# Kernel optimization log

Measured on AMD Instinct MI355X. Metric: run time of the kernel, lower is better.

The kernel has to match this reference:

```python
import jax, jax.numpy as jnp
import numpy as np

# Config mirrors Voxelization(__init__) with training=True -> max_voxels[0]
VOXEL_SIZE = (0.05, 0.05, 0.1)
PC_LO = (0.0, -40.0, -3.0)
PC_HI = (70.4, 40.0, 1.0)
MAX_POINTS = 64
MAX_VOXELS = 60000
GX = int(round((PC_HI[0] - PC_LO[0]) / VOXEL_SIZE[0]))  # 1408
GY = int(round((PC_HI[1] - PC_LO[1]) / VOXEL_SIZE[1]))  # 1600
GZ = int(round((PC_HI[2] - PC_LO[2]) / VOXEL_SIZE[2]))  # 40
SENT = GX * GY * GZ  # sentinel linear id for out-of-range points


def setup_inputs() -> dict:
    key = jax.random.key(0)
    u = jax.random.uniform(key, (2_000_000, 4), dtype=jnp.float32)
    lo = jnp.array([PC_LO[0], PC_LO[1], PC_LO[2], 0.0], jnp.float32)
    span = jnp.array([PC_HI[0] - PC_LO[0], PC_HI[1] - PC_LO[1], PC_HI[2] - PC_LO[2], 1.0], jnp.float32)
    points = lo + u * span  # xyz inside range, intensity in [0,1)
    return {"points": points}


def _voxelize(points):
    N, C = points.shape
    vs = jnp.array(VOXEL_SIZE, jnp.float32)
    lo = jnp.array(PC_LO, jnp.float32)
    grid = jnp.array([GX, GY, GZ], jnp.int32)

    g = jnp.floor((points[:, :3] - lo) / vs).astype(jnp.int32)  # [N,3] grid coords (x,y,z)
    valid = jnp.all((g >= 0) & (g < grid), axis=1)
    lin = (g[:, 0] * GY + g[:, 1]) * GZ + g[:, 2]
    lin = jnp.where(valid, lin, SENT).astype(jnp.int32)

    # Stable sort by voxel id; ties keep original point order (deterministic mode)
    order = jnp.argsort(lin)  # jnp.argsort is stable
    sl = lin[order]
    idx = jnp.arange(N, dtype=jnp.int32)
    is_start = jnp.concatenate([jnp.ones((1,), bool), sl[1:] != sl[:-1]])
    gid_sorted = (jnp.cumsum(is_start) - 1).astype(jnp.int32)  # sorted-group id per sorted point

    # First original point index per group -> first-occurrence voxel ordering
    group_first = jnp.full((N,), N, jnp.int32).at[gid_sorted].min(
        jnp.where(is_start, order.astype(jnp.int32), N))
    group_lin = jnp.full((N,), SENT, jnp.int32).at[gid_sorted].min(sl)
    group_first = jnp.where(group_lin == SENT, N, group_first)  # sentinel group ranks last
    perm = jnp.argsort(group_first)  # rank -> group
    inv_rank = jnp.zeros((N,), jnp.int32).at[perm].set(idx)  # group -> rank

    num_valid = jnp.sum(is_start & (sl != SENT)).astype(jnp.int32)
    voxel_num = jnp.minimum(num_valid, MAX_VOXELS)

    # Position within voxel (point order within group)
    start_idx = jax.lax.cummax(jnp.where(is_start, idx, -1))
    pos_sorted = idx - start_idx

    gid = jnp.zeros((N,), jnp.int32).at[order].set(gid_sorted)
    pos = jnp.zeros((N,), jnp.int32).at[order].set(pos_sorted)
    rank = inv_rank[gid]
    keep = valid & (rank < MAX_VOXELS) & (pos < MAX_POINTS)
    rk = jnp.where(keep, rank, MAX_VOXELS)  # OOB -> dropped
    pk = jnp.where(keep, pos, MAX_POINTS)

    voxels = jnp.zeros((MAX_VOXELS, MAX_POINTS, C), points.dtype).at[rk, pk].set(points, mode='drop')
    coors = jnp.zeros((MAX_VOXELS, 3), jnp.int32).at[rk].set(g[:, ::-1], mode='drop')  # flip -> (z,y,x)
    group_count = jnp.zeros((N,), jnp.int32).at[gid_sorted].add((sl != SENT).astype(jnp.int32))
    npv = jnp.minimum(group_count[perm], MAX_POINTS)[:MAX_VOXELS].astype(jnp.int32)
    return voxels, coors, npv, voxel_num


def reference(points):
    # Padded equivalent of torch output (voxels[:n], coors[:n].flip(-1), npv[:n]):
    # rows >= voxel_num are zero; voxel_num gives the true count.
    return _voxelize(points)
```

## Files before the change

### kernel.cpp

```cpp
#include <hip/hip_runtime.h>


#define MAXV 60000
#define MAXP 64
#define FCUT 131072
#define NBUCK 512
#define BSHIFT 13
#define BSLOTS 8192
#define TMASK (NBUCK * BSLOTS - 1)
#define BCAP 5120
#define ECAP 512
#define BIN_CHUNK 4096
#define BIN_T 512
#define NZ 512
#define CHUNK 2048
#define NCHUNK (FCUT / CHUNK)

typedef unsigned long long u64;

__device__ __forceinline__ int compute_lin(float x, float y, float z) {
  float fx = floorf((x - 0.0f) / 0.05f);
  float fy = floorf((y - (-40.0f)) / 0.05f);
  float fz = floorf((z - (-3.0f)) / 0.1f);
  if (!(fx >= 0.0f && fx < 1408.0f &&
        fy >= 0.0f && fy < 1600.0f &&
        fz >= 0.0f && fz < 40.0f))
    return -1;
  return (((int)fx) * 1600 + (int)fy) * 40 + (int)fz;
}

__device__ __forceinline__ unsigned hash_s(int lin) {
  unsigned h = (unsigned)lin * 2654435761u;
  return (h ^ (h >> 15)) & TMASK;
}

__global__ __launch_bounds__(BIN_T) void k_binA(
    const float4* __restrict__ pts, int N, u64* __restrict__ binned,
    int* __restrict__ bucketCnt, int nBin,
    float4* __restrict__ zOut, int nf4, float* __restrict__ zTail, int ntail,
    ulonglong2* __restrict__ zFs, int nfs2) {
  int tid = threadIdx.x;

  if (blockIdx.x >= nBin) {
    int gid = (blockIdx.x - nBin) * BIN_T + tid;
    int stride = NZ * BIN_T;
    float4 z = make_float4(0.f, 0.f, 0.f, 0.f);
    for (int i = gid; i < nf4; i += stride) zOut[i] = z;
    for (int i = gid; i < nfs2; i += stride) zFs[i] = make_ulonglong2(0, 0);
    if (gid < ntail) zTail[gid] = 0.f;
    return;
  }

  __shared__ int hist[NBUCK];
  __shared__ int lbase[NBUCK];
  __shared__ int cursor[NBUCK];
  __shared__ int gbase[NBUCK];
  __shared__ int totSh;
  __shared__ u64 stage[BIN_CHUNK];

  int blockStart = blockIdx.x * BIN_CHUNK;
  hist[tid] = 0;
  __syncthreads();

  unsigned sArr[8];
  int linArr[8];
#pragma unroll
  for (int j = 0; j < 8; j++) {
    int i = blockStart + j * BIN_T + tid;
    unsigned sv = 0xFFFFFFFFu; int lv = 0;
    if (i < N) {
      float4 p = pts[i];
      int lin = compute_lin(p.x, p.y, p.z);
      if (lin >= 0) {
        sv = hash_s(lin);
        lv = lin;
        atomicAdd(&hist[sv >> BSHIFT], 1);
      }
    }
    sArr[j] = sv; linArr[j] = lv;
  }
  __syncthreads();

  int v = hist[tid];
  lbase[tid] = v;
  __syncthreads();
  for (int off = 1; off < NBUCK; off <<= 1) {
    int t = (tid >= off) ? lbase[tid - off] : 0;
    __syncthreads();
    lbase[tid] += t;
    __syncthreads();
  }
  int excl = lbase[tid] - v;
  __syncthreads();
  lbase[tid] = excl;
  cursor[tid] = excl;
  __syncthreads();

#pragma unroll
  for (int j = 0; j < 8; j++) {
    if (sArr[j] != 0xFFFFFFFFu) {
      int b = (int)(sArr[j] >> BSHIFT);
      int k = atomicAdd(&cursor[b], 1);
      int i = blockStart + j * BIN_T + tid;
      stage[k] = ((u64)(unsigned)linArr[j] << 32) | (unsigned)i;
    }
  }
  __syncthreads();

  int cntB = cursor[tid] - lbase[tid];
  if (cntB > 0) gbase[tid] = atomicAdd(&bucketCnt[tid], cntB);
  if (tid == BIN_T - 1) totSh = cursor[NBUCK - 1];
  __syncthreads();

  int tot = totSh;
  for (int k = tid; k < tot; k += BIN_T) {
    u64 e = stage[k];
    int b = (int)(hash_s((int)(e >> 32)) >> BSHIFT);
    int off = gbase[b] + (k - lbase[b]);
    if (off < BCAP) binned[(size_t)b * BCAP + off] = e;
  }
}

__global__ __launch_bounds__(1024) void k_binB(
    const u64* __restrict__ binned, const int* __restrict__ bucketCnt,
    u64* __restrict__ fs, u64* __restrict__ gEbuf, int* __restrict__ bcnt,
    int* __restrict__ occPartials) {
  __shared__ u64 tab[BSLOTS];
  __shared__ u64 ev[ECAP];
  __shared__ int evCnt;
  __shared__ int occTot;

  int tid = threadIdx.x;
  int b = blockIdx.x;
  for (int k = tid; k < BSLOTS / 2; k += 1024)
    ((ulonglong2*)tab)[k] = make_ulonglong2(~0ull, ~0ull);
  if (tid == 0) { evCnt = 0; occTot = 0; }
  __syncthreads();

  int n = bucketCnt[b]; if (n > BCAP) n = BCAP;
  for (int k = tid; k < n; k += 1024) {
    u64 e = binned[(size_t)b * BCAP + k];
    int i = (int)(unsigned)e;
    int lin = (int)(e >> 32);
    int ls = (int)(hash_s(lin) & (BSLOTS - 1));
    u64 mine = ((u64)(unsigned)i << 40) | ((u64)(unsigned)lin << 12);
    for (;;) {
      u64 cur = atomicCAS(&tab[ls], ~0ull, mine);
      if (cur == ~0ull) break;
      if (((cur >> 12) & 0xFFFFFFFull) == (u64)(unsigned)lin) {
        for (;;) {
          unsigned f = (unsigned)(cur >> 40);
          unsigned c = (unsigned)(cur & 0xFFFu);
          unsigned nf = ((unsigned)i < f) ? (unsigned)i : f;
          unsigned rec = ((unsigned)i < f) ? f : (unsigned)i;
          unsigned nc = (c < 0xFFFu) ? c + 1 : 0xFFFu;
          u64 nv = ((u64)nf << 40) | ((u64)(unsigned)lin << 12) | nc;
          u64 prev = atomicCAS(&tab[ls], cur, nv);
          if (prev == cur) {
            unsigned pos = c + 1;
            if (pos < MAXP) {
              int eidx = atomicAdd(&evCnt, 1);
              if (eidx < ECAP)
                ev[eidx] = ((u64)ls << 40) | ((u64)pos << 24) | rec;
            }
            break;
          }
          cur = prev;
        }
        break;
      }
      ls = (ls + 1) & (BSLOTS - 1);
    }
  }
  __syncthreads();

  int ec = evCnt; if (ec > ECAP) ec = ECAP;
  for (int k = tid; k < ec; k += 1024) {
    u64 e = ev[k];
    int ls = (int)(e >> 40);
    u64 pm = (e >> 24) & 0xFFFFull;
    unsigned rec = (unsigned)(e & 0xFFFFFFu);
    unsigned f = (unsigned)(tab[ls] >> 40);
    gEbuf[(size_t)b * ECAP + k] =
        (f < FCUT) ? (((u64)f << 40) | (pm << 24) | rec) : ~0ull;
  }
  if (tid == 0) bcnt[b] = ec;

  int occ = 0;
  for (int k = tid; k < BSLOTS / 2; k += 1024) {
    ulonglong2 w2 = ((const ulonglong2*)tab)[k];
#pragma unroll
    for (int h = 0; h < 2; h++) {
      u64 w = h ? w2.y : w2.x;
      if (w != ~0ull) {
        occ++;
        unsigned f = (unsigned)(w >> 40);
        if (f < FCUT) {
          unsigned lin = (unsigned)((w >> 12) & 0xFFFFFFFull);
          unsigned c = (unsigned)(w & 0xFFFu) + 1;
          if (c > MAXP) c = MAXP;
          fs[f] = ((u64)lin << 8) | c;
        }
      }
    }
  }
  for (int off = 32; off > 0; off >>= 1) occ += __shfl_down(occ, off);
  if ((tid & 63) == 0) atomicAdd(&occTot, occ);
  __syncthreads();
  if (tid == 0) occPartials[b] = occTot;
}

__global__ __launch_bounds__(256) void k_rankLB(
    const u64* __restrict__ fs, const float4* __restrict__ pts,
    const int* __restrict__ occPartials, int* __restrict__ status,
    int* __restrict__ rankOf,
    float* __restrict__ outCoors, float* __restrict__ outNpv,
    float4* __restrict__ outVox, float* __restrict__ outNum,
    int* __restrict__ Dws) {
  int b = blockIdx.x;
  int tid = threadIdx.x;
  int base = b * CHUNK + tid * 8;
  __shared__ int sd[256];
  __shared__ int exclSh;

  u64 v[8];
  int sum = 0;
#pragma unroll
  for (int j = 0; j < 8; j++) {
    v[j] = fs[base + j];
    sum += (v[j] != 0) ? 1 : 0;
  }
  sd[tid] = sum;
  __syncthreads();
  for (int off = 1; off < 256; off <<= 1) {
    int t = (tid >= off) ? sd[tid - off] : 0;
    __syncthreads();
    sd[tid] += t;
    __syncthreads();
  }
  int inclThread = sd[tid];

  if (tid == 255)
    __hip_atomic_store(&status[b], 0x40000000 | inclThread,
                       __ATOMIC_RELEASE, __HIP_MEMORY_SCOPE_AGENT);

  int myAgg = 0;
  if (tid < b) {
    int sv;
    do {
      sv = __hip_atomic_load(&status[tid], __ATOMIC_ACQUIRE,
                             __HIP_MEMORY_SCOPE_AGENT);
    } while (!(sv & 0x40000000));
    myAgg = sv & 0x3FFFFFFF;
  }
  for (int off = 32; off > 0; off >>= 1) myAgg += __shfl_down(myAgg, off);
  if (tid == 0) exclSh = myAgg;
  __syncthreads();

  int run = exclSh + inclThread - sum;
#pragma unroll
  for (int j = 0; j < 8; j++) {
    if (v[j] != 0) {
      int f = base + j;
      int r = run++;
      rankOf[f] = r;
      if (r < MAXV) {
        int lin = (int)(v[j] >> 8);
        int gz = lin % 40;
        int t = lin / 40;
        int gy = t % 1600;
        int gx = t / 1600;
        outCoors[r * 3 + 0] = (float)gz;
        outCoors[r * 3 + 1] = (float)gy;
        outCoors[r * 3 + 2] = (float)gx;
        outNpv[r] = (float)(int)(v[j] & 0xFF);
        outVox[(size_t)r * MAXP] = pts[f];
      }
    }
  }

  if (b == 0) {
    int acc = 0;
    for (int i = tid; i < NBUCK; i += 256) acc += occPartials[i];
    __syncthreads();
    sd[tid] = acc;
    __syncthreads();
    for (int off = 128; off > 0; off >>= 1) {
      if (tid < off) sd[tid] += sd[tid + off];
      __syncthreads();
    }
    if (tid == 0) {
      int D = sd[0];
      int vn = D < MAXV ? D : MAXV;
      outNum[0] = (float)vn;
      Dws[0] = vn;
    }
  }
}

__global__ void k_events(const float4* __restrict__ pts,
                         const int* __restrict__ bcnt,
                         const u64* __restrict__ gEbuf,
                         const int* __restrict__ rankOf,
                         const int* __restrict__ Dws,
                         float* __restrict__ outCoors,
                         float* __restrict__ outNpv,
                         float4* __restrict__ outVox) {
  int gid = blockIdx.x * 256 + threadIdx.x;

  int D = Dws[0];
  for (int r = D + gid; r < MAXV; r += NBUCK * ECAP) {
    outCoors[r * 3 + 0] = 0.f; outCoors[r * 3 + 1] = 0.f;
    outCoors[r * 3 + 2] = 0.f; outNpv[r] = 0.f;
  }

  int b = gid >> 9;
  int t = gid & (ECAP - 1);
  if (t >= bcnt[b]) return;
  u64 e = gEbuf[(size_t)b * ECAP + t];
  if (e == ~0ull) return;
  unsigned f = (unsigned)(e >> 40);
  unsigned pos = (unsigned)((e >> 24) & 0xFFFFu);
  unsigned rec = (unsigned)(e & 0xFFFFFFu);
  int r = rankOf[f];
  if ((unsigned)r >= (unsigned)MAXV) return;
  outVox[(size_t)r * MAXP + pos] = pts[rec];
}

extern "C" void kernel_launch(void* const* d_in, const int* in_sizes, int n_in,
                              void* d_out, int out_size, void* d_ws, size_t ws_size,
                              hipStream_t stream) {
  const float4* pts = (const float4*)d_in[0];
  int N = in_sizes[0] / 4;

  float* out = (float*)d_out;
  float* outVox = out;
  float* outCoors = out + (size_t)MAXV * MAXP * 4;
  float* outNpv = outCoors + (size_t)MAXV * 3;
  float* outNum = outNpv + MAXV;

  char* w = (char*)d_ws;
  u64* binned = (u64*)w;         w += (size_t)NBUCK * BCAP * 8;
  u64* gEbuf = (u64*)w;          w += (size_t)NBUCK * ECAP * 8;
  int* rankOf = (int*)w;         w += (size_t)FCUT * 4;
  int* occPartials = (int*)w;    w += NBUCK * 4;
  int* bcnt = (int*)w;           w += NBUCK * 4;
  int* Dws = (int*)w;            w += 256;
  u64* fs = (u64*)w;             w += (size_t)FCUT * 8;
  char* z0 = w;
  int* bucketCnt = (int*)w;      w += NBUCK * 4;
  int* status = (int*)w;         w += NCHUNK * 4;
  size_t zBytes = (size_t)(w - z0);

  hipMemsetAsync(z0, 0, zBytes, stream);

  int nbA = (N + BIN_CHUNK - 1) / BIN_CHUNK;
  int nf4 = out_size >> 2;
  int ntail = out_size - (nf4 << 2);
  float* zTail = out + ((size_t)nf4 << 2);

  k_binA<<<nbA + NZ, BIN_T, 0, stream>>>(pts, N, binned, bucketCnt, nbA,
                                         (float4*)out, nf4, zTail, ntail,
                                         (ulonglong2*)fs, FCUT / 2);
  k_binB<<<NBUCK, 1024, 0, stream>>>(binned, bucketCnt, fs, gEbuf, bcnt,
                                     occPartials);
  k_rankLB<<<NCHUNK, 256, 0, stream>>>(fs, pts, occPartials, status, rankOf,
                                       outCoors, outNpv, (float4*)outVox,
                                       outNum, Dws);
  k_events<<<NBUCK * ECAP / 256, 256, 0, stream>>>(pts, bcnt, gEbuf, rankOf,
                                                   Dws, outCoors, outNpv,
                                                   (float4*)outVox);
}
```

Measured before the change: 134.3 us.

## Use wave shuffle scans and defer per-voxel output writes to events kernel

The shared-memory Hillis-Steele scans in the binning and ranking kernels become wavefront shuffle scans plus a small per-wave offset table, which cuts the number of block barriers. The ranking kernel no longer decodes coordinates or copies the first point. It stores a packed (point index, lin, count) record per rank in a new workspace array, and the events kernel writes coors, npv and the first voxel point from that array. This shortens the serial critical path of the decoupled-lookback scan kernel, at the cost of an extra 8-byte-per-voxel round trip through global memory.

```diff
diff --git a/kernel.cpp b/kernel.cpp
--- a/kernel.cpp
+++ b/kernel.cpp
@@ -55,7 +55,7 @@
   __shared__ int lbase[NBUCK];
   __shared__ int cursor[NBUCK];
   __shared__ int gbase[NBUCK];
-  __shared__ int totSh;
+  __shared__ int wsum8[8];
   __shared__ u64 stage[BIN_CHUNK];
 
   int blockStart = blockIdx.x * BIN_CHUNK;
@@ -82,16 +82,23 @@
   __syncthreads();
 
   int v = hist[tid];
-  lbase[tid] = v;
-  __syncthreads();
-  for (int off = 1; off < NBUCK; off <<= 1) {
-    int t = (tid >= off) ? lbase[tid - off] : 0;
-    __syncthreads();
-    lbase[tid] += t;
-    __syncthreads();
-  }
-  int excl = lbase[tid] - v;
-  __syncthreads();
+  int lane = tid & 63, wv = tid >> 6;
+  int x = v;
+#pragma unroll
+  for (int off = 1; off < 64; off <<= 1) {
+    int t = __shfl_up(x, off);
+    if (lane >= off) x += t;
+  }
+  if (lane == 63) wsum8[wv] = x;
+  __syncthreads();
+  int woff = 0, tot = 0;
+#pragma unroll
+  for (int w = 0; w < 8; w++) {
+    int s = wsum8[w];
+    tot += s;
+    woff += (w < wv) ? s : 0;
+  }
+  int excl = woff + x - v;
   lbase[tid] = excl;
   cursor[tid] = excl;
   __syncthreads();
@@ -109,10 +116,8 @@
 
   int cntB = cursor[tid] - lbase[tid];
   if (cntB > 0) gbase[tid] = atomicAdd(&bucketCnt[tid], cntB);
-  if (tid == BIN_T - 1) totSh = cursor[NBUCK - 1];
-  __syncthreads();
-
-  int tot = totSh;
+  __syncthreads();
+
   for (int k = tid; k < tot; k += BIN_T) {
     u64 e = stage[k];
     int b = (int)(hash_s((int)(e >> 32)) >> BSHIFT);
@@ -211,15 +216,14 @@
 }
 
 __global__ __launch_bounds__(256) void k_rankLB(
-    const u64* __restrict__ fs, const float4* __restrict__ pts,
-    const int* __restrict__ occPartials, int* __restrict__ status,
-    int* __restrict__ rankOf,
-    float* __restrict__ outCoors, float* __restrict__ outNpv,
-    float4* __restrict__ outVox, float* __restrict__ outNum,
+    const u64* __restrict__ fs, const int* __restrict__ occPartials,
+    int* __restrict__ status, int* __restrict__ rankOf,
+    u64* __restrict__ rankedF, float* __restrict__ outNum,
     int* __restrict__ Dws) {
   int b = blockIdx.x;
   int tid = threadIdx.x;
   int base = b * CHUNK + tid * 8;
+  __shared__ int wpart[4];
   __shared__ int sd[256];
   __shared__ int exclSh;
 
@@ -230,15 +234,20 @@
     v[j] = fs[base + j];
     sum += (v[j] != 0) ? 1 : 0;
   }
-  sd[tid] = sum;
-  __syncthreads();
-  for (int off = 1; off < 256; off <<= 1) {
-    int t = (tid >= off) ? sd[tid - off] : 0;
-    __syncthreads();
-    sd[tid] += t;
-    __syncthreads();
-  }
-  int inclThread = sd[tid];
+
+  int lane = tid & 63, wv = tid >> 6;
+  int x = sum;
+#pragma unroll
+  for (int off = 1; off < 64; off <<= 1) {
+    int t = __shfl_up(x, off);
+    if (lane >= off) x += t;
+  }
+  if (lane == 63) wpart[wv] = x;
+  __syncthreads();
+  int woff = 0;
+#pragma unroll
+  for (int w = 0; w < 4; w++) woff += (w < wv) ? wpart[w] : 0;
+  int inclThread = woff + x;
 
   if (tid == 255)
     __hip_atomic_store(&status[b], 0x40000000 | inclThread,
@@ -264,18 +273,8 @@
       int f = base + j;
       int r = run++;
       rankOf[f] = r;
-      if (r < MAXV) {
-        int lin = (int)(v[j] >> 8);
-        int gz = lin % 40;
-        int t = lin / 40;
-        int gy = t % 1600;
-        int gx = t / 1600;
-        outCoors[r * 3 + 0] = (float)gz;
-        outCoors[r * 3 + 1] = (float)gy;
-        outCoors[r * 3 + 2] = (float)gx;
-        outNpv[r] = (float)(int)(v[j] & 0xFF);
-        outVox[(size_t)r * MAXP] = pts[f];
-      }
+      if (r < MAXV)
+        rankedF[r] = ((u64)(unsigned)f << 35) | v[j];
     }
   }
 
@@ -303,12 +302,29 @@
                          const u64* __restrict__ gEbuf,
                          const int* __restrict__ rankOf,
                          const int* __restrict__ Dws,
+                         const u64* __restrict__ rankedF,
                          float* __restrict__ outCoors,
                          float* __restrict__ outNpv,
                          float4* __restrict__ outVox) {
   int gid = blockIdx.x * 256 + threadIdx.x;
-
   int D = Dws[0];
+
+  if (gid < D) {
+    u64 rec = rankedF[gid];
+    int f = (int)(rec >> 35);
+    int lin = (int)((rec >> 8) & 0x7FFFFFFull);
+    int cnt = (int)(rec & 0xFF);
+    int gz = lin % 40;
+    int t2 = lin / 40;
+    int gy = t2 % 1600;
+    int gx = t2 / 1600;
+    outCoors[gid * 3 + 0] = (float)gz;
+    outCoors[gid * 3 + 1] = (float)gy;
+    outCoors[gid * 3 + 2] = (float)gx;
+    outNpv[gid] = (float)cnt;
+    outVox[(size_t)gid * MAXP] = pts[f];
+  }
+
   for (int r = D + gid; r < MAXV; r += NBUCK * ECAP) {
     outCoors[r * 3 + 0] = 0.f; outCoors[r * 3 + 1] = 0.f;
     outCoors[r * 3 + 2] = 0.f; outNpv[r] = 0.f;
@@ -343,6 +359,7 @@
   u64* binned = (u64*)w;         w += (size_t)NBUCK * BCAP * 8;
   u64* gEbuf = (u64*)w;          w += (size_t)NBUCK * ECAP * 8;
   int* rankOf = (int*)w;         w += (size_t)FCUT * 4;
+  u64* rankedF = (u64*)w;        w += (size_t)MAXV * 8;
   int* occPartials = (int*)w;    w += NBUCK * 4;
   int* bcnt = (int*)w;           w += NBUCK * 4;
   int* Dws = (int*)w;            w += 256;
@@ -364,10 +381,9 @@
                                          (ulonglong2*)fs, FCUT / 2);
   k_binB<<<NBUCK, 1024, 0, stream>>>(binned, bucketCnt, fs, gEbuf, bcnt,
                                      occPartials);
-  k_rankLB<<<NCHUNK, 256, 0, stream>>>(fs, pts, occPartials, status, rankOf,
-                                       outCoors, outNpv, (float4*)outVox,
-                                       outNum, Dws);
+  k_rankLB<<<NCHUNK, 256, 0, stream>>>(fs, occPartials, status, rankOf,
+                                       rankedF, outNum, Dws);
   k_events<<<NBUCK * ECAP / 256, 256, 0, stream>>>(pts, bcnt, gEbuf, rankOf,
-                                                   Dws, outCoors, outNpv,
-                                                   (float4*)outVox);
-}
+                                                   Dws, rankedF, outCoors,
+                                                   outNpv, (float4*)outVox);
+}
```

Measured after the change: 133.3 us. Within noise of the previous version (-0.8%).
